# Performance work log

Hardware: AMD Instinct MI355X
Metric: run time of the kernel (lower is better)

## Reference

```python
import jax, jax.numpy as jnp
import numpy as np

B, T, F, U = 64, 512, 32, 64
EPS = 1e-3  # keras LayerNormalization default epsilon


def _ln(x, g, b):
    m = jnp.mean(x, axis=-1, keepdims=True)
    v = jnp.var(x, axis=-1, keepdims=True)
    return (x - m) / jnp.sqrt(v + EPS) * g + b


def setup_inputs() -> dict:
    key = jax.random.key(0)
    ks = jax.random.split(key, 24)
    s = 0.05
    inp = {
        "x": jax.random.normal(ks[0], (B, T, F), dtype=jnp.float32),
        # per-feature GRNs, stacked over F (each sub-net has independent params)
        "W1": jax.random.normal(ks[1], (F, U), jnp.float32) * s,   # dense_1 (1->U)
        "b1": jnp.zeros((F, U), jnp.float32),
        "W2": jax.random.normal(ks[2], (F, U, U), jnp.float32) * s,  # dense_2 (U->U)
        "b2": jnp.zeros((F, U), jnp.float32),
        "Wg1": jax.random.normal(ks[3], (F, U, U), jnp.float32) * s,  # GLU linear
        "bg1": jnp.zeros((F, U), jnp.float32),
        "Wg2": jax.random.normal(ks[4], (F, U, U), jnp.float32) * s,  # GLU gate
        "bg2": jnp.zeros((F, U), jnp.float32),
        "Wp": jax.random.normal(ks[5], (F, U), jnp.float32) * s,   # project (1->U)
        "bp": jnp.zeros((F, U), jnp.float32),
        "gamma": jnp.ones((F, U), jnp.float32),
        "beta": jnp.zeros((F, U), jnp.float32),
        # weights GRN (F -> F, no projection since in_dim == units == F)
        "w1w": jax.random.normal(ks[6], (F, F), jnp.float32) * s,
        "b1w": jnp.zeros((F,), jnp.float32),
        "w2w": jax.random.normal(ks[7], (F, F), jnp.float32) * s,
        "b2w": jnp.zeros((F,), jnp.float32),
        "wg1w": jax.random.normal(ks[8], (F, F), jnp.float32) * s,
        "bg1w": jnp.zeros((F,), jnp.float32),
        "wg2w": jax.random.normal(ks[9], (F, F), jnp.float32) * s,
        "bg2w": jnp.zeros((F,), jnp.float32),
        "gammaw": jnp.ones((F,), jnp.float32),
        "betaw": jnp.zeros((F,), jnp.float32),
    }
    return inp


def reference(x, W1, b1, W2, b2, Wg1, bg1, Wg2, bg2, Wp, bp, gamma, beta,
              w1w, b1w, w2w, b2w, wg1w, bg1w, wg2w, bg2w, gammaw, betaw):
    # ---- variable weights GRN on flattened features (input dim F == units F, no projection) ----
    h = jax.nn.elu(jnp.einsum('btf,fg->btg', x, w1w) + b1w)
    h = jnp.einsum('btf,fg->btg', h, w2w) + b2w
    g = (jnp.einsum('btf,fg->btg', h, wg1w) + bg1w) * jax.nn.sigmoid(
        jnp.einsum('btf,fg->btg', h, wg2w) + bg2w)
    w = _ln(g + x, gammaw, betaw)
    w = jax.nn.softmax(w, axis=-1)  # [B,T,F]

    # ---- per-feature GRNs, batched over F (scalar input per feature) ----
    xe = x[..., None]                                   # [B,T,F,1]
    res = xe * Wp + bp                                  # project residual [B,T,F,U]
    h = jax.nn.elu(xe * W1 + b1)                        # dense_1 [B,T,F,U]
    h = jnp.einsum('btfu,fuv->btfv', h, W2) + b2        # dense_2
    g = (jnp.einsum('btfu,fuv->btfv', h, Wg1) + bg1) * jax.nn.sigmoid(
        jnp.einsum('btfu,fuv->btfv', h, Wg2) + bg2)     # GLU
    y = _ln(g + res, gamma, beta)                       # [B,T,F,U]

    out = jnp.einsum('btfu,btf->btu', y, w)             # softmax-weighted sum over features
    return out, w
```

## Files before the change

### kernel.cpp

```cpp
#include <hip/hip_runtime.h>


typedef float f4      __attribute__((ext_vector_type(4)));
typedef float f32x4   __attribute__((ext_vector_type(4)));
typedef short bf16x8  __attribute__((ext_vector_type(8)));

#define N_ROWS 32768
#define F_DIM  32
#define U_DIM  64
#define RPB    128
#define NTHR   512
#define NBLK   (N_ROWS / RPB)

#define X_OFF   0
#define WT_OFF  18432
#define WB_OFF  35328
#define VB_OFF  84480
#define H2_OFF  89088
#define SMEM_BYTES 123904

__device__ __forceinline__ unsigned short f2bf(float x) {
  union { float f; unsigned u; } c; c.f = x;
  unsigned r = (c.u + 0x7FFFu + ((c.u >> 16) & 1u)) >> 16;
  return (unsigned short)r;
}

__global__ __launch_bounds__(256) void vsn_prep(
    const float* __restrict__ W2,  const float* __restrict__ Wg1, const float* __restrict__ Wg2,
    const float* __restrict__ W1,  const float* __restrict__ b1,  const float* __restrict__ b2,
    const float* __restrict__ bg1, const float* __restrict__ bg2,
    const float* __restrict__ Wp,  const float* __restrict__ bp,
    const float* __restrict__ gamma_, const float* __restrict__ beta_,
    unsigned short* __restrict__ wtg, float* __restrict__ vect)
{
  const int t = threadIdx.x, blk = blockIdx.x;
  if (blk < 96) {
    __shared__ float tile[64][65];
    const int m = blk >> 5, f = blk & 31;
    const float* src = (m == 0) ? W2 : (m == 1) ? Wg1 : Wg2;
    src += f * 4096;
    #pragma unroll
    for (int i = 0; i < 16; ++i) {
      int idx = t + i * 256;
      tile[idx >> 6][idx & 63] = src[idx];
    }
    __syncthreads();
    unsigned short* dst = wtg + (m * 32 + f) * 4096;
    #pragma unroll
    for (int i = 0; i < 16; ++i) {
      int idx = t + i * 256;
      dst[idx] = f2bf(tile[idx & 63][idx >> 6]);
    }
  } else {
    #pragma unroll
    for (int a = 0; a < 9; ++a) {
      const float* s = (a==0)?W1:(a==1)?b1:(a==2)?b2:(a==3)?bg1:(a==4)?bg2:
                       (a==5)?Wp:(a==6)?bp:(a==7)?gamma_:beta_;
      for (int i = t; i < 2048; i += 256)
        vect[(i >> 6) * 576 + a * 64 + (i & 63)] = s[i];
    }
  }
}

__global__ __launch_bounds__(NTHR, 2) void vsn_main(
    const float* __restrict__ x,
    const unsigned short* __restrict__ wtg,
    const float* __restrict__ vect,
    const float* __restrict__ w1w, const float* __restrict__ w2w,
    const float* __restrict__ wg1w, const float* __restrict__ wg2w,
    const float* __restrict__ b1w, const float* __restrict__ b2w,
    const float* __restrict__ bg1w, const float* __restrict__ bg2w,
    const float* __restrict__ gammaw, const float* __restrict__ betaw,
    float* __restrict__ out, float* __restrict__ wout)
{
  __shared__ __align__(16) char smem[SMEM_BYTES];
  const int t  = threadIdx.x;
  const int r0 = blockIdx.x * RPB;

  float* xt  = (float*)(smem + X_OFF);
  float* wtl = (float*)(smem + WT_OFF);
  unsigned short* wbuf = (unsigned short*)(smem + WB_OFF);
  float* vbuf = (float*)(smem + VB_OFF);
  float* h2b  = (float*)(smem + H2_OFF);
  float* wAl = (float*)(smem + WB_OFF);
  float* vAl = (float*)(smem + WB_OFF + 16384);
  float* hex = (float*)(smem + H2_OFF);

  #pragma unroll
  for (int i = 0; i < 2; ++i) {
    int i4 = t + i * NTHR;
    f4 v = ((const f4*)(x + (size_t)r0 * F_DIM))[i4];
    *((f4*)(xt + (i4 >> 3) * 36 + ((i4 & 7) << 2))) = v;
  }

  int4 pw0, pw1, pw2; f4 pv0;
  {
    const int4* wt4 = (const int4*)wtg;
    pw0 = wt4[(0 * 32 + 0) * 512 + t];
    pw1 = wt4[(1 * 32 + 0) * 512 + t];
    pw2 = wt4[(2 * 32 + 0) * 512 + t];
    if (t < 144) pv0 = ((const f4*)(vect))[t];
  }

  #pragma unroll
  for (int i = 0; i < 2; ++i) {
    int i4 = t + i * NTHR;
    int m = i4 >> 8, off = (i4 & 255) << 2;
    const float* src = (m == 0) ? w1w : (m == 1) ? w2w : (m == 2) ? wg1w : wg2w;
    *(f4*)(wAl + m * 1024 + off) = *((const f4*)(src + off));
  }
  if (t < 48) {
    int m = t >> 3, off = (t & 7) << 2;
    const float* src = (m==0)?b1w:(m==1)?b2w:(m==2)?bg1w:(m==3)?bg2w:(m==4)?gammaw:betaw;
    *(f4*)(vAl + m * 32 + off) = *((const f4*)(src + off));
  }
  __syncthreads();

  {
    const int ar = t >> 2;
    const int g0 = (t & 3) << 3;

    float hacc[8];
    #pragma unroll
    for (int j = 0; j < 8; ++j) hacc[j] = vAl[0 * 32 + g0 + j];
    #pragma unroll
    for (int ff = 0; ff < 32; ++ff) {
      float xv = xt[ar * 36 + ff];
      f4 w0 = *(const f4*)(wAl + 0 * 1024 + ff * 32 + g0);
      f4 w1 = *(const f4*)(wAl + 0 * 1024 + ff * 32 + g0 + 4);
      #pragma unroll
      for (int j = 0; j < 4; ++j) { hacc[j] += xv * w0[j]; hacc[4 + j] += xv * w1[j]; }
    }
    #pragma unroll
    for (int j = 0; j < 8; ++j) { float z = hacc[j]; hacc[j] = z > 0.f ? z : (__expf(z) - 1.f); }
    *(f4*)(hex + ar * 36 + g0)     = (f4){hacc[0], hacc[1], hacc[2], hacc[3]};
    *(f4*)(hex + ar * 36 + g0 + 4) = (f4){hacc[4], hacc[5], hacc[6], hacc[7]};
    __syncthreads();

    float h2acc[8];
    #pragma unroll
    for (int j = 0; j < 8; ++j) h2acc[j] = vAl[1 * 32 + g0 + j];
    #pragma unroll
    for (int ff = 0; ff < 32; ++ff) {
      float hv = hex[ar * 36 + ff];
      f4 w0 = *(const f4*)(wAl + 1 * 1024 + ff * 32 + g0);
      f4 w1 = *(const f4*)(wAl + 1 * 1024 + ff * 32 + g0 + 4);
      #pragma unroll
      for (int j = 0; j < 4; ++j) { h2acc[j] += hv * w0[j]; h2acc[4 + j] += hv * w1[j]; }
    }
    __syncthreads();
    *(f4*)(hex + ar * 36 + g0)     = (f4){h2acc[0], h2acc[1], h2acc[2], h2acc[3]};
    *(f4*)(hex + ar * 36 + g0 + 4) = (f4){h2acc[4], h2acc[5], h2acc[6], h2acc[7]};
    __syncthreads();

    float aacc[8], bacc[8];
    #pragma unroll
    for (int j = 0; j < 8; ++j) { aacc[j] = vAl[2 * 32 + g0 + j]; bacc[j] = vAl[3 * 32 + g0 + j]; }
    #pragma unroll
    for (int ff = 0; ff < 32; ++ff) {
      float hv = hex[ar * 36 + ff];
      f4 wa0 = *(const f4*)(wAl + 2 * 1024 + ff * 32 + g0);
      f4 wa1 = *(const f4*)(wAl + 2 * 1024 + ff * 32 + g0 + 4);
      f4 wb0 = *(const f4*)(wAl + 3 * 1024 + ff * 32 + g0);
      f4 wb1 = *(const f4*)(wAl + 3 * 1024 + ff * 32 + g0 + 4);
      #pragma unroll
      for (int j = 0; j < 4; ++j) {
        aacc[j] += hv * wa0[j]; aacc[4 + j] += hv * wa1[j];
        bacc[j] += hv * wb0[j]; bacc[4 + j] += hv * wb1[j];
      }
    }
    float zz[8];
    #pragma unroll
    for (int j = 0; j < 8; ++j) {
      float sg = __builtin_amdgcn_rcpf(1.f + __expf(-bacc[j]));
      zz[j] = aacc[j] * sg + xt[ar * 36 + g0 + j];
    }
    __syncthreads();
    *(f4*)(hex + ar * 36 + g0)     = (f4){zz[0], zz[1], zz[2], zz[3]};
    *(f4*)(hex + ar * 36 + g0 + 4) = (f4){zz[4], zz[5], zz[6], zz[7]};
    __syncthreads();

    float s1 = 0.f, s2 = 0.f;
    #pragma unroll
    for (int ff = 0; ff < 32; ++ff) { float z = hex[ar * 36 + ff]; s1 += z; s2 += z * z; }
    float mA = s1 * 0.03125f;
    float vA = s2 * 0.03125f - mA * mA;
    float rsA = __builtin_amdgcn_rsqf(vA + 1e-3f);
    float mx = -1e30f;
    #pragma unroll
    for (int ff = 0; ff < 32; ++ff) {
      float y = (hex[ar * 36 + ff] - mA) * rsA * vAl[4 * 32 + ff] + vAl[5 * 32 + ff];
      mx = fmaxf(mx, y);
    }
    float es = 0.f;
    #pragma unroll
    for (int ff = 0; ff < 32; ++ff) {
      float y = (hex[ar * 36 + ff] - mA) * rsA * vAl[4 * 32 + ff] + vAl[5 * 32 + ff];
      es += __expf(y - mx);
    }
    float inv = __builtin_amdgcn_rcpf(es);
    float wv8[8];
    #pragma unroll
    for (int j = 0; j < 8; ++j) {
      float y = (hex[ar * 36 + g0 + j] - mA) * rsA * vAl[4 * 32 + g0 + j] + vAl[5 * 32 + g0 + j];
      wv8[j] = __expf(y - mx) * inv;
      wtl[ar * 33 + g0 + j] = wv8[j];
    }
    *(f4*)(wout + (size_t)(r0 + ar) * 32 + g0)     = (f4){wv8[0], wv8[1], wv8[2], wv8[3]};
    *(f4*)(wout + (size_t)(r0 + ar) * 32 + g0 + 4) = (f4){wv8[4], wv8[5], wv8[6], wv8[7]};
    __syncthreads();
  }

  {
    const int bo = t * 16;
    const int sw = bo ^ (((t >> 3) & 7) << 4);
    char* wb0 = (char*)wbuf;
    *(int4*)(wb0 + 0 * 8192 + sw) = pw0;
    *(int4*)(wb0 + 1 * 8192 + sw) = pw1;
    *(int4*)(wb0 + 2 * 8192 + sw) = pw2;
    if (t < 144) *(f4*)(vbuf + t * 4) = pv0;
  }
  __syncthreads();

  const int wid = t >> 6;
  const int lr  = t & 15;
  const int lg  = (t >> 4) & 3;
  float* h2w = h2b + wid * (16 * 68);

  f32x4 acc[4];
  #pragma unroll
  for (int nt = 0; nt < 4; ++nt) acc[nt] = (f32x4){0.f, 0.f, 0.f, 0.f};

  int cur = 0;
  for (int f = 0; f < F_DIM; ++f) {
    int4 qw0, qw1, qw2; f4 qv;
    if (f < 31) {
      const int4* wt4 = (const int4*)wtg;
      qw0 = wt4[(0 * 32 + f + 1) * 512 + t];
      qw1 = wt4[(1 * 32 + f + 1) * 512 + t];
      qw2 = wt4[(2 * 32 + f + 1) * 512 + t];
      if (t < 144) qv = ((const f4*)(vect + (f + 1) * 576))[t];
    }

    const char*  wbc = (const char*)wbuf + cur * 24576;
    const float* vbc = vbuf + cur * 576;

    const float s_ = xt[(wid * 16 + lr) * 36 + f];
    bf16x8 afr[2];
    #pragma unroll
    for (int kt = 0; kt < 2; ++kt) {
      const int u0 = 8 * lg + 32 * kt;
      f4 wa  = *(const f4*)(vbc + u0);
      f4 wb_ = *(const f4*)(vbc + u0 + 4);
      f4 ba  = *(const f4*)(vbc + 64 + u0);
      f4 bb_ = *(const f4*)(vbc + 64 + u0 + 4);
      bf16x8 af;
      #pragma unroll
      for (int j = 0; j < 4; ++j) {
        float h = s_ * wa[j] + ba[j];
        h = h > 0.f ? h : (__expf(h) - 1.f);
        af[j] = (short)f2bf(h);
      }
      #pragma unroll
      for (int j = 0; j < 4; ++j) {
        float h = s_ * wb_[j] + bb_[j];
        h = h > 0.f ? h : (__expf(h) - 1.f);
        af[4 + j] = (short)f2bf(h);
      }
      afr[kt] = af;
    }

    f32x4 c1[4];
    #pragma unroll
    for (int nt = 0; nt < 4; ++nt) {
      c1[nt] = (f32x4){0.f, 0.f, 0.f, 0.f};
      const int v_ = lr + 16 * nt;
      #pragma unroll
      for (int kt = 0; kt < 2; ++kt) {
        int bo = (v_ << 7) + ((8 * lg + 32 * kt) << 1);
        bo ^= (v_ & 7) << 4;
        bf16x8 bfr = *(const bf16x8*)(wbc + 0 * 8192 + bo);
        c1[nt] = __builtin_amdgcn_mfma_f32_16x16x32_bf16(afr[kt], bfr, c1[nt], 0, 0, 0);
      }
    }

    #pragma unroll
    for (int nt = 0; nt < 4; ++nt) {
      const float b2v = vbc[2 * 64 + lr + 16 * nt];
      #pragma unroll
      for (int rg = 0; rg < 4; ++rg)
        h2w[(4 * lg + rg) * 68 + lr + 16 * nt] = c1[nt][rg] + b2v;
    }
    asm volatile("s_waitcnt lgkmcnt(0)" ::: "memory");

    bf16x8 a2[2];
    #pragma unroll
    for (int kt = 0; kt < 2; ++kt) {
      const int u0 = 8 * lg + 32 * kt;
      f4 p0 = *(const f4*)(h2w + lr * 68 + u0);
      f4 p1 = *(const f4*)(h2w + lr * 68 + u0 + 4);
      bf16x8 af;
      #pragma unroll
      for (int j = 0; j < 4; ++j) { af[j] = (short)f2bf(p0[j]); af[4 + j] = (short)f2bf(p1[j]); }
      a2[kt] = af;
    }

    f32x4 ca[4], cb[4];
    #pragma unroll
    for (int nt = 0; nt < 4; ++nt) { ca[nt] = (f32x4){0.f,0.f,0.f,0.f}; cb[nt] = (f32x4){0.f,0.f,0.f,0.f}; }
    #pragma unroll
    for (int nt = 0; nt < 4; ++nt) {
      const int v_ = lr + 16 * nt;
      #pragma unroll
      for (int kt = 0; kt < 2; ++kt) {
        int bo = (v_ << 7) + ((8 * lg + 32 * kt) << 1);
        bo ^= (v_ & 7) << 4;
        bf16x8 b1f = *(const bf16x8*)(wbc + 1 * 8192 + bo);
        bf16x8 b2f = *(const bf16x8*)(wbc + 2 * 8192 + bo);
        ca[nt] = __builtin_amdgcn_mfma_f32_16x16x32_bf16(a2[kt], b1f, ca[nt], 0, 0, 0);
        cb[nt] = __builtin_amdgcn_mfma_f32_16x16x32_bf16(a2[kt], b2f, cb[nt], 0, 0, 0);
      }
    }

    float xr[4], wr[4];
    #pragma unroll
    for (int rg = 0; rg < 4; ++rg) {
      const int rl = wid * 16 + 4 * lg + rg;
      xr[rg] = xt[rl * 36 + f];
      wr[rg] = wtl[rl * 33 + f];
    }
    float zf[4][4];
    float s1[4] = {0.f,0.f,0.f,0.f}, s2[4] = {0.f,0.f,0.f,0.f};
    #pragma unroll
    for (int nt = 0; nt < 4; ++nt) {
      const int u = lr + 16 * nt;
      const float bg1v = vbc[3 * 64 + u], bg2v = vbc[4 * 64 + u];
      const float wpv  = vbc[5 * 64 + u], bpv  = vbc[6 * 64 + u];
      #pragma unroll
      for (int rg = 0; rg < 4; ++rg) {
        float a = ca[nt][rg] + bg1v;
        float b = cb[nt][rg] + bg2v;
        float sg = __builtin_amdgcn_rcpf(1.f + __expf(-b));
        float z = a * sg + (xr[rg] * wpv + bpv);
        zf[nt][rg] = z;
        s1[rg] += z;
        s2[rg] += z * z;
      }
    }
    #pragma unroll
    for (int rg = 0; rg < 4; ++rg) {
      #pragma unroll
      for (int m = 1; m < 16; m <<= 1) {
        s1[rg] += __shfl_xor(s1[rg], m, 64);
        s2[rg] += __shfl_xor(s2[rg], m, 64);
      }
    }
    float mn[4], rs[4];
    #pragma unroll
    for (int rg = 0; rg < 4; ++rg) {
      mn[rg] = s1[rg] * 0.015625f;
      float var = s2[rg] * 0.015625f - mn[rg] * mn[rg];
      rs[rg] = __builtin_amdgcn_rsqf(var + 1e-3f);
    }
    #pragma unroll
    for (int nt = 0; nt < 4; ++nt) {
      const int u = lr + 16 * nt;
      const float gav = vbc[7 * 64 + u], bev = vbc[8 * 64 + u];
      #pragma unroll
      for (int rg = 0; rg < 4; ++rg) {
        float y = (zf[nt][rg] - mn[rg]) * rs[rg] * gav + bev;
        acc[nt][rg] += y * wr[rg];
      }
    }

    if (f < 31) {
      const int bo = t * 16;
      const int sw = bo ^ (((t >> 3) & 7) << 4);
      char* wbn = (char*)wbuf + (cur ^ 1) * 24576;
      *(int4*)(wbn + 0 * 8192 + sw) = qw0;
      *(int4*)(wbn + 1 * 8192 + sw) = qw1;
      *(int4*)(wbn + 2 * 8192 + sw) = qw2;
      if (t < 144) *(f4*)(vbuf + (cur ^ 1) * 576 + t * 4) = qv;
      cur ^= 1;
    }
    __syncthreads();
  }

  #pragma unroll
  for (int nt = 0; nt < 4; ++nt) {
    #pragma unroll
    for (int rg = 0; rg < 4; ++rg) {
      const int row = r0 + wid * 16 + 4 * lg + rg;
      out[(size_t)row * U_DIM + lr + 16 * nt] = acc[nt][rg];
    }
  }
}

extern "C" void kernel_launch(void* const* d_in, const int* in_sizes, int n_in,
                              void* d_out, int out_size, void* d_ws, size_t ws_size,
                              hipStream_t stream)
{
  (void)in_sizes; (void)n_in; (void)out_size; (void)ws_size;
  const float* x    = (const float*)d_in[0];
  const float* W1   = (const float*)d_in[1];
  const float* b1   = (const float*)d_in[2];
  const float* W2   = (const float*)d_in[3];
  const float* b2   = (const float*)d_in[4];
  const float* Wg1  = (const float*)d_in[5];
  const float* bg1  = (const float*)d_in[6];
  const float* Wg2  = (const float*)d_in[7];
  const float* bg2  = (const float*)d_in[8];
  const float* Wp   = (const float*)d_in[9];
  const float* bp   = (const float*)d_in[10];
  const float* gm   = (const float*)d_in[11];
  const float* bt   = (const float*)d_in[12];
  const float* w1w  = (const float*)d_in[13];
  const float* b1w  = (const float*)d_in[14];
  const float* w2w  = (const float*)d_in[15];
  const float* b2w  = (const float*)d_in[16];
  const float* wg1w = (const float*)d_in[17];
  const float* bg1w = (const float*)d_in[18];
  const float* wg2w = (const float*)d_in[19];
  const float* bg2w = (const float*)d_in[20];
  const float* gmw  = (const float*)d_in[21];
  const float* btw  = (const float*)d_in[22];

  unsigned short* wtg = (unsigned short*)d_ws;
  float* vect = (float*)((char*)d_ws + 786432);

  float* out  = (float*)d_out;
  float* wout = out + (size_t)N_ROWS * U_DIM;

  vsn_prep<<<97, 256, 0, stream>>>(W2, Wg1, Wg2, W1, b1, b2, bg1, bg2, Wp, bp, gm, bt, wtg, vect);
  vsn_main<<<NBLK, NTHR, 0, stream>>>(x, wtg, vect, w1w, w2w, wg1w, wg2w,
                                      b1w, b2w, bg1w, bg2w, gmw, btw, out, wout);
}
```

Measured before the change: 219.2 us.

## Halve block size to 64 rows and store intermediates in LDS as bf16

Each block now covers 64 rows with 256 threads instead of 128 rows with 512, which shrinks LDS use so more blocks can reside per CU. The GRN hidden activations and softmax weights are written to LDS as bf16 instead of fp32, so the MFMA A operand loads directly with no per-element conversion. Each thread now issues two weight loads per matrix per feature, and the whole weight set is streamed per block, so twice as many blocks means twice the weight traffic. Storing the softmax weights in bf16 also lowers the precision of the final weighted sum.

```diff
diff --git a/kernel.cpp b/kernel.cpp
--- a/kernel.cpp
+++ b/kernel.cpp
@@ -1,28 +1,33 @@
 #include <hip/hip_runtime.h>
+#include <hip/hip_bf16.h>
 
 
 typedef float f4      __attribute__((ext_vector_type(4)));
 typedef float f32x4   __attribute__((ext_vector_type(4)));
 typedef short bf16x8  __attribute__((ext_vector_type(8)));
+typedef unsigned short u16x8 __attribute__((ext_vector_type(8)));
 
 #define N_ROWS 32768
 #define F_DIM  32
 #define U_DIM  64
-#define RPB    128
-#define NTHR   512
+#define RPB    64
+#define NTHR   256
 #define NBLK   (N_ROWS / RPB)
 
 #define X_OFF   0
-#define WT_OFF  18432
-#define WB_OFF  35328
-#define VB_OFF  84480
-#define H2_OFF  89088
-#define SMEM_BYTES 123904
-
-__device__ __forceinline__ unsigned short f2bf(float x) {
-  union { float f; unsigned u; } c; c.f = x;
-  unsigned r = (c.u + 0x7FFFu + ((c.u >> 16) & 1u)) >> 16;
-  return (unsigned short)r;
+#define WT_OFF  9216
+#define WB_OFF  14336
+#define VB_OFF  63488
+#define H2_OFF  68096
+#define SMEM_BYTES 77312
+
+__device__ __forceinline__ unsigned short bfu(float x) {
+  union { __hip_bfloat16 h; unsigned short u; } c;
+  c.h = __float2bfloat16(x);
+  return c.u;
+}
+__device__ __forceinline__ float bf2f(unsigned short u) {
+  union { float f; unsigned v; } c; c.v = ((unsigned)u) << 16; return c.f;
 }
 
 __global__ __launch_bounds__(256) void vsn_prep(
@@ -49,7 +54,7 @@
     #pragma unroll
     for (int i = 0; i < 16; ++i) {
       int idx = t + i * 256;
-      dst[idx] = f2bf(tile[idx & 63][idx >> 6]);
+      dst[idx] = bfu(tile[idx & 63][idx >> 6]);
     }
   } else {
     #pragma unroll
@@ -78,10 +83,10 @@
   const int r0 = blockIdx.x * RPB;
 
   float* xt  = (float*)(smem + X_OFF);
-  float* wtl = (float*)(smem + WT_OFF);
+  unsigned short* wtlb = (unsigned short*)(smem + WT_OFF);
   unsigned short* wbuf = (unsigned short*)(smem + WB_OFF);
   float* vbuf = (float*)(smem + VB_OFF);
-  float* h2b  = (float*)(smem + H2_OFF);
+  unsigned short* h2b = (unsigned short*)(smem + H2_OFF);
   float* wAl = (float*)(smem + WB_OFF);
   float* vAl = (float*)(smem + WB_OFF + 16384);
   float* hex = (float*)(smem + H2_OFF);
@@ -93,17 +98,20 @@
     *((f4*)(xt + (i4 >> 3) * 36 + ((i4 & 7) << 2))) = v;
   }
 
-  int4 pw0, pw1, pw2; f4 pv0;
+  int4 pw0[2], pw1[2], pw2[2]; f4 pv0;
   {
     const int4* wt4 = (const int4*)wtg;
-    pw0 = wt4[(0 * 32 + 0) * 512 + t];
-    pw1 = wt4[(1 * 32 + 0) * 512 + t];
-    pw2 = wt4[(2 * 32 + 0) * 512 + t];
+    #pragma unroll
+    for (int j = 0; j < 2; ++j) {
+      pw0[j] = wt4[(0 * 32 + 0) * 512 + t + j * 256];
+      pw1[j] = wt4[(1 * 32 + 0) * 512 + t + j * 256];
+      pw2[j] = wt4[(2 * 32 + 0) * 512 + t + j * 256];
+    }
     if (t < 144) pv0 = ((const f4*)(vect))[t];
   }
 
   #pragma unroll
-  for (int i = 0; i < 2; ++i) {
+  for (int i = 0; i < 4; ++i) {
     int i4 = t + i * NTHR;
     int m = i4 >> 8, off = (i4 & 255) << 2;
     const float* src = (m == 0) ? w1w : (m == 1) ? w2w : (m == 2) ? wg1w : wg2w;
@@ -200,24 +208,29 @@
     }
     float inv = __builtin_amdgcn_rcpf(es);
     float wv8[8];
+    u16x8 wu;
     #pragma unroll
     for (int j = 0; j < 8; ++j) {
       float y = (hex[ar * 36 + g0 + j] - mA) * rsA * vAl[4 * 32 + g0 + j] + vAl[5 * 32 + g0 + j];
       wv8[j] = __expf(y - mx) * inv;
-      wtl[ar * 33 + g0 + j] = wv8[j];
-    }
+      wu[j] = bfu(wv8[j]);
+    }
+    *(u16x8*)(wtlb + ar * 40 + g0) = wu;
     *(f4*)(wout + (size_t)(r0 + ar) * 32 + g0)     = (f4){wv8[0], wv8[1], wv8[2], wv8[3]};
     *(f4*)(wout + (size_t)(r0 + ar) * 32 + g0 + 4) = (f4){wv8[4], wv8[5], wv8[6], wv8[7]};
     __syncthreads();
   }
 
   {
-    const int bo = t * 16;
-    const int sw = bo ^ (((t >> 3) & 7) << 4);
-    char* wb0 = (char*)wbuf;
-    *(int4*)(wb0 + 0 * 8192 + sw) = pw0;
-    *(int4*)(wb0 + 1 * 8192 + sw) = pw1;
-    *(int4*)(wb0 + 2 * 8192 + sw) = pw2;
+    #pragma unroll
+    for (int j = 0; j < 2; ++j) {
+      const int p = t + j * 256;
+      const int sw = (p * 16) ^ (((p >> 3) & 7) << 4);
+      char* wb0 = (char*)wbuf;
+      *(int4*)(wb0 + 0 * 8192 + sw) = pw0[j];
+      *(int4*)(wb0 + 1 * 8192 + sw) = pw1[j];
+      *(int4*)(wb0 + 2 * 8192 + sw) = pw2[j];
+    }
     if (t < 144) *(f4*)(vbuf + t * 4) = pv0;
   }
   __syncthreads();
@@ -225,7 +238,7 @@
   const int wid = t >> 6;
   const int lr  = t & 15;
   const int lg  = (t >> 4) & 3;
-  float* h2w = h2b + wid * (16 * 68);
+  unsigned short* h2w = h2b + wid * (16 * 72);
 
   f32x4 acc[4];
   #pragma unroll
@@ -233,12 +246,15 @@
 
   int cur = 0;
   for (int f = 0; f < F_DIM; ++f) {
-    int4 qw0, qw1, qw2; f4 qv;
+    int4 qw0[2], qw1[2], qw2[2]; f4 qv;
     if (f < 31) {
       const int4* wt4 = (const int4*)wtg;
-      qw0 = wt4[(0 * 32 + f + 1) * 512 + t];
-      qw1 = wt4[(1 * 32 + f + 1) * 512 + t];
-      qw2 = wt4[(2 * 32 + f + 1) * 512 + t];
+      #pragma unroll
+      for (int j = 0; j < 2; ++j) {
+        qw0[j] = wt4[(0 * 32 + f + 1) * 512 + t + j * 256];
+        qw1[j] = wt4[(1 * 32 + f + 1) * 512 + t + j * 256];
+        qw2[j] = wt4[(2 * 32 + f + 1) * 512 + t + j * 256];
+      }
       if (t < 144) qv = ((const f4*)(vect + (f + 1) * 576))[t];
     }
 
@@ -259,13 +275,13 @@
       for (int j = 0; j < 4; ++j) {
         float h = s_ * wa[j] + ba[j];
         h = h > 0.f ? h : (__expf(h) - 1.f);
-        af[j] = (short)f2bf(h);
+        af[j] = (short)bfu(h);
       }
       #pragma unroll
       for (int j = 0; j < 4; ++j) {
         float h = s_ * wb_[j] + bb_[j];
         h = h > 0.f ? h : (__expf(h) - 1.f);
-        af[4 + j] = (short)f2bf(h);
+        af[4 + j] = (short)bfu(h);
       }
       afr[kt] = af;
     }
@@ -289,21 +305,14 @@
       const float b2v = vbc[2 * 64 + lr + 16 * nt];
       #pragma unroll
       for (int rg = 0; rg < 4; ++rg)
-        h2w[(4 * lg + rg) * 68 + lr + 16 * nt] = c1[nt][rg] + b2v;
+        h2w[(4 * lg + rg) * 72 + lr + 16 * nt] = bfu(c1[nt][rg] + b2v);
     }
     asm volatile("s_waitcnt lgkmcnt(0)" ::: "memory");
 
     bf16x8 a2[2];
     #pragma unroll
-    for (int kt = 0; kt < 2; ++kt) {
-      const int u0 = 8 * lg + 32 * kt;
-      f4 p0 = *(const f4*)(h2w + lr * 68 + u0);
-      f4 p1 = *(const f4*)(h2w + lr * 68 + u0 + 4);
-      bf16x8 af;
-      #pragma unroll
-      for (int j = 0; j < 4; ++j) { af[j] = (short)f2bf(p0[j]); af[4 + j] = (short)f2bf(p1[j]); }
-      a2[kt] = af;
-    }
+    for (int kt = 0; kt < 2; ++kt)
+      a2[kt] = *(const bf16x8*)(h2w + lr * 72 + 8 * lg + 32 * kt);
 
     f32x4 ca[4], cb[4];
     #pragma unroll
@@ -327,7 +336,7 @@
     for (int rg = 0; rg < 4; ++rg) {
       const int rl = wid * 16 + 4 * lg + rg;
       xr[rg] = xt[rl * 36 + f];
-      wr[rg] = wtl[rl * 33 + f];
+      wr[rg] = bf2f(wtlb[rl * 40 + f]);
     }
     float zf[4][4];
     float s1[4] = {0.f,0.f,0.f,0.f}, s2[4] = {0.f,0.f,0.f,0.f};
@@ -374,12 +383,15 @@
     }
 
     if (f < 31) {
-      const int bo = t * 16;
-      const int sw = bo ^ (((t >> 3) & 7) << 4);
       char* wbn = (char*)wbuf + (cur ^ 1) * 24576;
-      *(int4*)(wbn + 0 * 8192 + sw) = qw0;
-      *(int4*)(wbn + 1 * 8192 + sw) = qw1;
-      *(int4*)(wbn + 2 * 8192 + sw) = qw2;
+      #pragma unroll
+      for (int j = 0; j < 2; ++j) {
+        const int p = t + j * 256;
+        const int sw = (p * 16) ^ (((p >> 3) & 7) << 4);
+        *(int4*)(wbn + 0 * 8192 + sw) = qw0[j];
+        *(int4*)(wbn + 1 * 8192 + sw) = qw1[j];
+        *(int4*)(wbn + 2 * 8192 + sw) = qw2[j];
+      }
       if (t < 144) *(f4*)(vbuf + (cur ^ 1) * 576 + t * 4) = qv;
       cur ^= 1;
     }
```

Result: slower. 227.0 us (+3.6%).
